# Performance work log

Measured on AMD Instinct MI355X. Metric: run time of the kernel, lower is better.

The kernel has to match this reference:

```python
import jax, jax.numpy as jnp
import numpy as np

B, N, DIM = 4, 4096, 512
HEADS, DH = 8, 64          # dim_head = dim // 8
M = 256                    # num_landmarks = dim // 2
ITERS = 6                  # pinv iterations
K = 33                     # residual depthwise conv kernel
INNER = HEADS * DH


def setup_inputs() -> dict:
    key = jax.random.key(0)
    ks = jax.random.split(key, 7)
    return {
        "x": jax.random.normal(ks[0], (B, N, DIM), jnp.float32),
        "norm_w": 1.0 + 0.02 * jax.random.normal(ks[1], (DIM,), jnp.float32),
        "norm_b": 0.02 * jax.random.normal(ks[2], (DIM,), jnp.float32),
        "w_qkv": jax.random.normal(ks[3], (DIM, 3 * INNER), jnp.float32) / np.sqrt(DIM),
        "w_out": jax.random.normal(ks[4], (INNER, DIM), jnp.float32) / np.sqrt(INNER),
        "b_out": 0.02 * jax.random.normal(ks[5], (DIM,), jnp.float32),
        "res_w": jax.random.normal(ks[6], (HEADS, 1, K, 1), jnp.float32) / np.sqrt(K),
    }


def _moore_penrose_pinv(x, iters):
    # iterative Newton-Schulz pseudoinverse, as in lucidrains nystrom-attention
    abs_x = jnp.abs(x)
    col = abs_x.sum(-1)
    row = abs_x.sum(-2)
    z = jnp.swapaxes(x, -1, -2) / (jnp.max(col) * jnp.max(row))
    I = jnp.eye(x.shape[-1], dtype=x.dtype)
    for _ in range(iters):
        xz = x @ z
        z = 0.25 * z @ (13.0 * I - xz @ (15.0 * I - xz @ (7.0 * I - xz)))
    return z


def reference(x, norm_w, norm_b, w_qkv, w_out, b_out, res_w):
    # LayerNorm (eps=1e-5, torch default)
    mu = x.mean(-1, keepdims=True)
    var = ((x - mu) ** 2).mean(-1, keepdims=True)
    xn = (x - mu) / jnp.sqrt(var + 1e-5) * norm_w + norm_b

    qkv = xn @ w_qkv                               # [B,N,3*INNER]
    q, k, v = jnp.split(qkv, 3, axis=-1)
    to_heads = lambda t: t.reshape(B, N, HEADS, DH).transpose(0, 2, 1, 3)  # [B,H,N,D]
    q, k, v = to_heads(q), to_heads(k), to_heads(v)
    q = q * (DH ** -0.5)

    # landmarks: mean over consecutive blocks of l = N // M tokens
    l = N // M
    q_l = q.reshape(B, HEADS, M, l, DH).mean(3)    # [B,H,M,D]
    k_l = k.reshape(B, HEADS, M, l, DH).mean(3)

    sim1 = jnp.einsum('bhid,bhjd->bhij', q, k_l)   # [B,H,N,M]
    sim2 = jnp.einsum('bhid,bhjd->bhij', q_l, k_l) # [B,H,M,M]
    sim3 = jnp.einsum('bhid,bhjd->bhij', q_l, k)   # [B,H,M,N]
    a1 = jax.nn.softmax(sim1, -1)
    a2 = jax.nn.softmax(sim2, -1)
    a3 = jax.nn.softmax(sim3, -1)

    a2_inv = _moore_penrose_pinv(a2, ITERS)
    out = (a1 @ a2_inv) @ (a3 @ v)                 # [B,H,N,D]

    # residual depthwise conv over sequence dim (Conv2d(h,h,(33,1),groups=h))
    out = out + jax.lax.conv_general_dilated(
        v, res_w, (1, 1), ((K // 2, K // 2), (0, 0)),
        feature_group_count=HEADS,
        dimension_numbers=('NCHW', 'OIHW', 'NCHW'))

    out = out.transpose(0, 2, 1, 3).reshape(B, N, INNER)
    out = out @ w_out + b_out                      # to_out (dropout inactive at eval)
    return x + out                                 # TransLayer residual
```

## Files before the change

### kernel.cpp

```cpp
#include <hip/hip_runtime.h>
#include <math.h>

typedef unsigned short u16;
typedef short s16x8 __attribute__((ext_vector_type(8)));
typedef float f32x4 __attribute__((ext_vector_type(4)));

#define MFMA16(a, b, c) __builtin_amdgcn_mfma_f32_16x16x32_bf16((a), (b), (c), 0, 0, 0)

__device__ __forceinline__ u16 f2b(float f) {
  unsigned u = __float_as_uint(f);
  unsigned r = (u + 0x7fff + ((u >> 16) & 1)) >> 16;
  return (u16)r;
}
__device__ __forceinline__ float b2f(u16 h) { return __uint_as_float(((unsigned)h) << 16); }

__global__ __launch_bounds__(256) void ln_kernel(const float* __restrict__ x, const float* __restrict__ w,
                          const float* __restrict__ b, u16* __restrict__ xn) {
  int row = blockIdx.x;
  const float* xr = x + (size_t)row * 512;
  int t = threadIdx.x;
  float v0 = xr[t], v1 = xr[t + 256];
  float s = v0 + v1, ss = v0*v0 + v1*v1;
  for (int o = 32; o > 0; o >>= 1) { s += __shfl_down(s, o); ss += __shfl_down(ss, o); }
  __shared__ float ls[4], lss[4];
  int wid = t >> 6, lane = t & 63;
  if (lane == 0) { ls[wid] = s; lss[wid] = ss; }
  __syncthreads();
  float tot  = ls[0]+ls[1]+ls[2]+ls[3];
  float tot2 = lss[0]+lss[1]+lss[2]+lss[3];
  float mean = tot * (1.f/512);
  float var  = tot2 * (1.f/512) - mean*mean;
  float inv = rsqrtf(var + 1e-5f);
  u16* xo = xn + (size_t)row * 512;
  xo[t]     = f2b((v0-mean)*inv*w[t]     + b[t]);
  xo[t+256] = f2b((v1-mean)*inv*w[t+256] + b[t+256]);
}

__global__ __launch_bounds__(256) void wcast_T(const float* __restrict__ W, u16* __restrict__ WT, int R, int C) {
  int idx = blockIdx.x*256 + threadIdx.x;
  if (idx >= R*C) return;
  int r = idx / C, c = idx - r*C;
  WT[(size_t)c*R + r] = f2b(W[idx]);
}

__global__ __launch_bounds__(256) void vtrans(const u16* __restrict__ v, u16* __restrict__ vT) {
  __shared__ u16 tile[64][72];
  int bh = blockIdx.y, n0 = blockIdx.x * 64;
  int t = threadIdx.x;
  const u16* vb = v + ((size_t)bh*4096 + n0)*64;
  #pragma unroll
  for (int p = 0; p < 2; p++) {
    int c = t + p*256;
    int r = c >> 3, col = (c & 7)*8;
    *(uint4*)&tile[r][col] = *(const uint4*)&vb[(size_t)r*64 + col];
  }
  __syncthreads();
  #pragma unroll
  for (int p = 0; p < 2; p++) {
    int c = t + p*256;
    int d = c >> 3, ncol = (c & 7)*8;
    u16 tmp[8];
    #pragma unroll
    for (int j = 0; j < 8; j++) tmp[j] = tile[ncol + j][d];
    *(uint4*)&vT[((size_t)bh*64 + d)*4096 + n0 + ncol] = *(uint4*)tmp;
  }
}

__device__ __forceinline__ void gemm128_core(const u16* __restrict__ A, const u16* __restrict__ BT,
    int K, int ldA, int ldBT, int row0, int col0, u16* As, u16* Bs, f32x4 acc[4][4]) {
  int t = threadIdx.x, lane = t & 63, wid = t >> 6;
  int wr = (wid >> 1) * 64, wc = (wid & 1) * 64;
  int lr = lane & 15, lg = lane >> 4;
  for (int k0 = 0; k0 < K; k0 += 32) {
    __syncthreads();
    #pragma unroll
    for (int p = 0; p < 2; p++) {
      int ch = t + p*256;
      int r = ch >> 2, c = (ch & 3) * 8;
      *(uint4*)&As[r*40 + c] = *(const uint4*)&A[(size_t)(row0 + r)*ldA + k0 + c];
      *(uint4*)&Bs[r*40 + c] = *(const uint4*)&BT[(size_t)(col0 + r)*ldBT + k0 + c];
    }
    __syncthreads();
    s16x8 af[4], bf[4];
    #pragma unroll
    for (int f = 0; f < 4; f++) {
      af[f] = *(s16x8*)&As[(wr + f*16 + lr)*40 + lg*8];
      bf[f] = *(s16x8*)&Bs[(wc + f*16 + lr)*40 + lg*8];
    }
    #pragma unroll
    for (int i = 0; i < 4; i++)
      #pragma unroll
      for (int j = 0; j < 4; j++)
        acc[i][j] = MFMA16(af[i], bf[j], acc[i][j]);
  }
}

__device__ __forceinline__ void gemm_128x64_core(const u16* __restrict__ A, const u16* __restrict__ BT,
    int row0, int col0, u16* As, u16* Bs, f32x4 acc[4][2]) {
  int t = threadIdx.x, lane = t & 63, wid = t >> 6;
  int wr = (wid >> 1) * 64, wc = (wid & 1) * 32;
  int lr = lane & 15, lg = lane >> 4;
  for (int k0 = 0; k0 < 256; k0 += 32) {
    __syncthreads();
    #pragma unroll
    for (int p = 0; p < 2; p++) {
      int ch = t + p*256;
      int r = ch >> 2, c = (ch & 3) * 8;
      *(uint4*)&As[r*40 + c] = *(const uint4*)&A[(size_t)(row0 + r)*256 + k0 + c];
    }
    { int r = t >> 2, c = (t & 3) * 8;
      *(uint4*)&Bs[r*40 + c] = *(const uint4*)&BT[(size_t)(col0 + r)*256 + k0 + c]; }
    __syncthreads();
    s16x8 af[4], bf[2];
    #pragma unroll
    for (int f = 0; f < 4; f++) af[f] = *(s16x8*)&As[(wr + f*16 + lr)*40 + lg*8];
    #pragma unroll
    for (int f = 0; f < 2; f++) bf[f] = *(s16x8*)&Bs[(wc + f*16 + lr)*40 + lg*8];
    #pragma unroll
    for (int i = 0; i < 4; i++)
      #pragma unroll
      for (int j = 0; j < 2; j++)
        acc[i][j] = MFMA16(af[i], bf[j], acc[i][j]);
  }
}

__global__ __launch_bounds__(256) void qkv_mfma(const u16* __restrict__ xn, const u16* __restrict__ wT,
    u16* __restrict__ q, u16* __restrict__ k, u16* __restrict__ v) {
  __shared__ u16 As[128*40], Bs[128*40];
  f32x4 acc[4][4];
  #pragma unroll
  for (int i = 0; i < 4; i++)
    #pragma unroll
    for (int j = 0; j < 4; j++) acc[i][j] = (f32x4)0.f;
  int bI = blockIdx.x;
  int job = (bI & 7)*192 + (bI >> 3);
  int row0 = (job / 12) * 128, col0 = (job % 12) * 128;
  gemm128_core(xn, wT, 512, 512, 512, row0, col0, As, Bs, acc);
  int t = threadIdx.x, lane = t & 63, wid = t >> 6, lr = lane & 15, lg = lane >> 4;
  int wr = (wid >> 1)*64, wc = (wid & 1)*64;
  #pragma unroll
  for (int i = 0; i < 4; i++)
    #pragma unroll
    for (int j = 0; j < 4; j++)
      #pragma unroll
      for (int r = 0; r < 4; r++) {
        int row = row0 + wr + i*16 + lg*4 + r;
        int col = col0 + wc + j*16 + lr;
        float val = acc[i][j][r];
        int part = col >> 9, rem = col & 511, h = rem >> 6, d = rem & 63;
        int b = row >> 12, n = row & 4095;
        size_t bh = (size_t)(b*8 + h);
        size_t dst = (bh*4096 + n)*64 + d;
        if (part == 0)      q[dst] = f2b(val * 0.125f);
        else if (part == 1) k[dst] = f2b(val);
        else                v[dst] = f2b(val);
      }
}

__global__ __launch_bounds__(256) void out_mfma(const u16* __restrict__ outh, const u16* __restrict__ wT,
    const float* __restrict__ bo, const float* __restrict__ x, float* __restrict__ out) {
  __shared__ u16 As[128*40], Bs[128*40];
  f32x4 acc[4][4];
  #pragma unroll
  for (int i = 0; i < 4; i++)
    #pragma unroll
    for (int j = 0; j < 4; j++) acc[i][j] = (f32x4)0.f;
  int bI = blockIdx.x;
  int job = (bI & 7)*64 + (bI >> 3);
  int row0 = (job / 4) * 128, col0 = (job % 4) * 128;
  gemm128_core(outh, wT, 512, 512, 512, row0, col0, As, Bs, acc);
  int t = threadIdx.x, lane = t & 63, wid = t >> 6, lr = lane & 15, lg = lane >> 4;
  int wr = (wid >> 1)*64, wc = (wid & 1)*64;
  #pragma unroll
  for (int i = 0; i < 4; i++)
    #pragma unroll
    for (int j = 0; j < 4; j++)
      #pragma unroll
      for (int r = 0; r < 4; r++) {
        int row = row0 + wr + i*16 + lg*4 + r;
        int col = col0 + wc + j*16 + lr;
        size_t idx = (size_t)row*512 + col;
        out[idx] = x[idx] + acc[i][j][r] + bo[col];
      }
}

__global__ __launch_bounds__(256) void pinv_s1(const u16* __restrict__ a2h, const u16* __restrict__ zcT,
    u16* __restrict__ xz, u16* __restrict__ xzT, u16* __restrict__ e1T) {
  __shared__ u16 As[128*40], Bs[64*40];
  size_t bb = (size_t)blockIdx.z << 16;
  f32x4 acc[4][2];
  #pragma unroll
  for (int i = 0; i < 4; i++) { acc[i][0] = (f32x4)0.f; acc[i][1] = (f32x4)0.f; }
  int row0 = blockIdx.y*128, col0 = blockIdx.x*64;
  gemm_128x64_core(a2h + bb, zcT + bb, row0, col0, As, Bs, acc);
  int t = threadIdx.x, lane = t & 63, wid = t >> 6, lr = lane & 15, lg = lane >> 4;
  int wr = (wid >> 1)*64, wc = (wid & 1)*32;
  #pragma unroll
  for (int i = 0; i < 4; i++)
    #pragma unroll
    for (int j = 0; j < 2; j++)
      #pragma unroll
      for (int r = 0; r < 4; r++) {
        int row = row0 + wr + i*16 + lg*4 + r;
        int col = col0 + wc + j*16 + lr;
        float c = acc[i][j][r];
        xz [bb + (size_t)row*256 + col] = f2b(c);
        xzT[bb + (size_t)col*256 + row] = f2b(c);
        e1T[bb + (size_t)col*256 + row] = f2b((row == col ? 7.f : 0.f) - c);
      }
}

__global__ __launch_bounds__(256) void pinv_s2(const u16* __restrict__ xz, const u16* __restrict__ e1T,
    const u16* __restrict__ zc, const u16* __restrict__ xzT,
    u16* __restrict__ e2T, u16* __restrict__ W) {
  __shared__ u16 As[128*40], Bs[64*40];
  int bz = blockIdx.z;
  bool isQ = bz < 32;
  size_t bb = (size_t)(isQ ? bz : bz - 32) << 16;
  const u16* Aptr = (isQ ? xz : zc) + bb;
  const u16* Bptr = (isQ ? e1T : xzT) + bb;
  f32x4 acc[4][2];
  #pragma unroll
  for (int i = 0; i < 4; i++) { acc[i][0] = (f32x4)0.f; acc[i][1] = (f32x4)0.f; }
  int row0 = blockIdx.y*128, col0 = blockIdx.x*64;
  gemm_128x64_core(Aptr, Bptr, row0, col0, As, Bs, acc);
  int t = threadIdx.x, lane = t & 63, wid = t >> 6, lr = lane & 15, lg = lane >> 4;
  int wr = (wid >> 1)*64, wc = (wid & 1)*32;
  #pragma unroll
  for (int i = 0; i < 4; i++)
    #pragma unroll
    for (int j = 0; j < 2; j++)
      #pragma unroll
      for (int r = 0; r < 4; r++) {
        int row = row0 + wr + i*16 + lg*4 + r;
        int col = col0 + wc + j*16 + lr;
        float c = acc[i][j][r];
        if (isQ) e2T[bb + (size_t)col*256 + row] = f2b((row == col ? 15.f : 0.f) - c);
        else     W  [bb + (size_t)row*256 + col] = f2b(c);
      }
}

__global__ __launch_bounds__(256) void pinv_s3(const u16* __restrict__ W, const u16* __restrict__ e2T,
    const u16* __restrict__ zc, u16* __restrict__ zn, u16* __restrict__ znT) {
  __shared__ u16 As[128*40], Bs[64*40];
  size_t bb = (size_t)blockIdx.z << 16;
  f32x4 acc[4][2];
  #pragma unroll
  for (int i = 0; i < 4; i++) { acc[i][0] = (f32x4)0.f; acc[i][1] = (f32x4)0.f; }
  int row0 = blockIdx.y*128, col0 = blockIdx.x*64;
  gemm_128x64_core(W + bb, e2T + bb, row0, col0, As, Bs, acc);
  int t = threadIdx.x, lane = t & 63, wid = t >> 6, lr = lane & 15, lg = lane >> 4;
  int wr = (wid >> 1)*64, wc = (wid & 1)*32;
  #pragma unroll
  for (int i = 0; i < 4; i++)
    #pragma unroll
    for (int j = 0; j < 2; j++)
      #pragma unroll
      for (int r = 0; r < 4; r++) {
        int row = row0 + wr + i*16 + lg*4 + r;
        int col = col0 + wc + j*16 + lr;
        size_t idx = bb + (size_t)row*256 + col;
        float val = 3.25f*b2f(zc[idx]) - 0.25f*acc[i][j][r];
        zn [idx] = f2b(val);
        znT[bb + (size_t)col*256 + row] = f2b(val);
      }
}

__global__ __launch_bounds__(256) void bmm64(const u16* __restrict__ A, const u16* __restrict__ BT,
    u16* __restrict__ Cn, u16* __restrict__ CT, u16* __restrict__ CE,
    int M, int N, int K, float alpha, float diag) {
  __shared__ u16 As[64*40], Bs[64*40];
  int batch = blockIdx.z;
  const u16* Ab = A  + (size_t)batch*M*K;
  const u16* Bb = BT + (size_t)batch*N*K;
  int row0 = blockIdx.y*64, col0 = blockIdx.x*64;
  int t = threadIdx.x, lane = t & 63, wid = t >> 6, lr = lane & 15, lg = lane >> 4;
  int wr = (wid >> 1)*32, wc = (wid & 1)*32;
  f32x4 acc[2][2];
  #pragma unroll
  for (int i = 0; i < 2; i++)
    #pragma unroll
    for (int j = 0; j < 2; j++) acc[i][j] = (f32x4)0.f;
  for (int k0 = 0; k0 < K; k0 += 32) {
    __syncthreads();
    int r = t >> 2, c = (t & 3)*8;
    *(uint4*)&As[r*40 + c] = *(const uint4*)&Ab[(size_t)(row0 + r)*K + k0 + c];
    *(uint4*)&Bs[r*40 + c] = *(const uint4*)&Bb[(size_t)(col0 + r)*K + k0 + c];
    __syncthreads();
    s16x8 af[2], bf[2];
    #pragma unroll
    for (int f = 0; f < 2; f++) {
      af[f] = *(s16x8*)&As[(wr + f*16 + lr)*40 + lg*8];
      bf[f] = *(s16x8*)&Bs[(wc + f*16 + lr)*40 + lg*8];
    }
    #pragma unroll
    for (int i = 0; i < 2; i++)
      #pragma unroll
      for (int j = 0; j < 2; j++)
        acc[i][j] = MFMA16(af[i], bf[j], acc[i][j]);
  }
  size_t cb = (size_t)batch*M*N;
  #pragma unroll
  for (int i = 0; i < 2; i++)
    #pragma unroll
    for (int j = 0; j < 2; j++)
      #pragma unroll
      for (int r = 0; r < 4; r++) {
        int row = row0 + wr + i*16 + lg*4 + r;
        int col = col0 + wc + j*16 + lr;
        float val = alpha*acc[i][j][r] + (row == col ? diag : 0.f);
        if (Cn) Cn[cb + (size_t)row*N + col] = f2b(val);
        if (CT) CT[cb + (size_t)col*M + row] = f2b(val);
        if (CE) CE[cb + (size_t)col*M + row] = f2b((row == col ? 7.f : 0.f) - val);
      }
}

__global__ void landmark_kernel(const u16* __restrict__ q, const u16* __restrict__ k,
                                u16* __restrict__ ql, u16* __restrict__ kl) {
  int idx = blockIdx.x;
  int d = threadIdx.x;
  size_t base = ((size_t)idx * 16) * 64 + d;
  float sq = 0.f, sk = 0.f;
  #pragma unroll
  for (int j = 0; j < 16; j++) { sq += b2f(q[base + (size_t)j*64]); sk += b2f(k[base + (size_t)j*64]); }
  ql[(size_t)idx*64 + d] = f2b(sq * (1.f/16.f));
  kl[(size_t)idx*64 + d] = f2b(sk * (1.f/16.f));
}

__global__ __launch_bounds__(256) void sim2_mfma(const u16* __restrict__ ql, const u16* __restrict__ kl,
    float* __restrict__ a2, u16* __restrict__ a2h, unsigned* __restrict__ scal) {
  __shared__ u16 Qs[256*72];
  __shared__ u16 Ks2[256*72];
  __shared__ float wcol[4*256];
  __shared__ float red[256];
  int bh = blockIdx.x;
  int t = threadIdx.x, lane = t & 63, wid = t >> 6, lr = lane & 15, lg = lane >> 4;
  #pragma unroll
  for (int p = 0; p < 8; p++) {
    int c = t + p*256;
    int r = c >> 3, col = (c & 7)*8;
    *(uint4*)&Qs[r*72 + col]  = *(const uint4*)&ql[((size_t)bh*256 + r)*64 + col];
    *(uint4*)&Ks2[r*72 + col] = *(const uint4*)&kl[((size_t)bh*256 + r)*64 + col];
  }
  __syncthreads();
  float colp[16];
  #pragma unroll
  for (int cf = 0; cf < 16; cf++) colp[cf] = 0.f;
  for (int rf = 0; rf < 4; rf++) {
    int rbase = wid*64 + rf*16;
    s16x8 a0 = *(s16x8*)&Qs[(rbase + lr)*72 + lg*8];
    s16x8 a1 = *(s16x8*)&Qs[(rbase + lr)*72 + 32 + lg*8];
    f32x4 sf[16];
    #pragma unroll
    for (int cf = 0; cf < 16; cf++) {
      s16x8 b0 = *(s16x8*)&Ks2[(cf*16 + lr)*72 + lg*8];
      s16x8 b1 = *(s16x8*)&Ks2[(cf*16 + lr)*72 + 32 + lg*8];
      sf[cf] = MFMA16(a1, b1, MFMA16(a0, b0, (f32x4)0.f));
    }
    #pragma unroll
    for (int r = 0; r < 4; r++) {
      float mx = -3e38f;
      #pragma unroll
      for (int cf = 0; cf < 16; cf++) mx = fmaxf(mx, sf[cf][r]);
      #pragma unroll
      for (int o = 1; o < 16; o <<= 1) mx = fmaxf(mx, __shfl_xor(mx, o));
      float sum = 0.f;
      #pragma unroll
      for (int cf = 0; cf < 16; cf++) { sf[cf][r] = __expf(sf[cf][r] - mx); sum += sf[cf][r]; }
      #pragma unroll
      for (int o = 1; o < 16; o <<= 1) sum += __shfl_xor(sum, o);
      float inv = 1.f / sum;
      int row = rbase + lg*4 + r;
      size_t base = (size_t)bh*65536 + (size_t)row*256;
      #pragma unroll
      for (int cf = 0; cf < 16; cf++) {
        float pp = sf[cf][r] * inv;
        a2[base + cf*16 + lr] = pp;
        a2h[base + cf*16 + lr] = f2b(pp);
        colp[cf] += pp;
      }
    }
  }
  #pragma unroll
  for (int cf = 0; cf < 16; cf++) {
    colp[cf] += __shfl_xor(colp[cf], 16);
    colp[cf] += __shfl_xor(colp[cf], 32);
  }
  if (lg == 0) {
    #pragma unroll
    for (int cf = 0; cf < 16; cf++) wcol[wid*256 + cf*16 + lr] = colp[cf];
  }
  __syncthreads();
  red[t] = wcol[t] + wcol[256 + t] + wcol[512 + t] + wcol[768 + t];
  __syncthreads();
  for (int o = 128; o > 0; o >>= 1) {
    if (t < o) red[t] = fmaxf(red[t], red[t+o]);
    __syncthreads();
  }
  if (t == 0) atomicMax(scal + 1, __float_as_uint(red[0]));
}

__global__ void z0_kernel(const float* __restrict__ a2, const unsigned* __restrict__ scal,
                          u16* __restrict__ zA, u16* __restrict__ zAT) {
  size_t idx = (size_t)blockIdx.x*256 + threadIdx.x;
  float inv = 1.f / __uint_as_float(scal[1]);
  size_t bh = idx >> 16; int rem = (int)(idx & 65535); int i = rem >> 8, j = rem & 255;
  zA[idx]  = f2b(a2[(bh<<16) + ((size_t)j<<8) + i] * inv);
  zAT[idx] = f2b(a2[idx] * inv);
}

__global__ __launch_bounds__(256) void flash_part(const u16* __restrict__ Q, const u16* __restrict__ Kg,
    const u16* __restrict__ VT, float* __restrict__ po, float* __restrict__ pm, float* __restrict__ pl) {
  __shared__ u16 Ks[64*72];
  __shared__ u16 Vs[64*72];
  __shared__ u16 Ps[4*16*72];
  int qt = blockIdx.x, ch = blockIdx.y, bh = blockIdx.z;
  int q0 = qt * 64;
  int t = threadIdx.x, lane = t & 63, wid = t >> 6, lr = lane & 15, lg = lane >> 4;
  const u16* Qb  = Q  + ((size_t)bh*256)*64;
  const u16* Kb  = Kg + ((size_t)bh*4096 + ch*512)*64;
  const u16* VTb = VT + ((size_t)bh*64)*4096 + ch*512;
  int qrow = q0 + wid*16 + lr;
  s16x8 aq0 = *(const s16x8*)&Qb[(size_t)qrow*64 + lg*8];
  s16x8 aq1 = *(const s16x8*)&Qb[(size_t)qrow*64 + 32 + lg*8];
  f32x4 oacc[4];
  #pragma unroll
  for (int f = 0; f < 4; f++) oacc[f] = (f32x4)0.f;
  float m_[4] = {-3e38f, -3e38f, -3e38f, -3e38f};
  float l_[4] = {0.f, 0.f, 0.f, 0.f};
  u16* Pw = Ps + wid*16*72;
  for (int k0 = 0; k0 < 512; k0 += 64) {
    __syncthreads();
    #pragma unroll
    for (int p = 0; p < 2; p++) {
      int c = t + p*256; int r = c >> 3, cc = (c & 7)*8;
      *(uint4*)&Ks[r*72 + cc] = *(const uint4*)&Kb[(size_t)(k0 + r)*64 + cc];
      *(uint4*)&Vs[r*72 + cc] = *(const uint4*)&VTb[(size_t)r*4096 + k0 + cc];
    }
    __syncthreads();
    f32x4 sf[4];
    #pragma unroll
    for (int f = 0; f < 4; f++) {
      s16x8 b0 = *(s16x8*)&Ks[(f*16 + lr)*72 + lg*8];
      s16x8 b1 = *(s16x8*)&Ks[(f*16 + lr)*72 + 32 + lg*8];
      f32x4 s = (f32x4)0.f;
      s = MFMA16(aq0, b0, s);
      s = MFMA16(aq1, b1, s);
      sf[f] = s;
    }
    #pragma unroll
    for (int r = 0; r < 4; r++) {
      float mx = fmaxf(fmaxf(sf[0][r], sf[1][r]), fmaxf(sf[2][r], sf[3][r]));
      #pragma unroll
      for (int o = 1; o < 16; o <<= 1) mx = fmaxf(mx, __shfl_xor(mx, o));
      float mn = fmaxf(m_[r], mx);
      float sum = 0.f;
      #pragma unroll
      for (int f = 0; f < 4; f++) {
        float pv = __expf(sf[f][r] - mn);
        sum += pv;
        Pw[(lg*4 + r)*72 + f*16 + lr] = f2b(pv);
      }
      #pragma unroll
      for (int o = 1; o < 16; o <<= 1) sum += __shfl_xor(sum, o);
      float sc = __expf(m_[r] - mn);
      l_[r] = l_[r]*sc + sum;
      m_[r] = mn;
      #pragma unroll
      for (int f = 0; f < 4; f++) oacc[f][r] *= sc;
    }
    __syncthreads();
    #pragma unroll
    for (int ks = 0; ks < 2; ks++) {
      s16x8 ap = *(s16x8*)&Pw[lr*72 + ks*32 + lg*8];
      #pragma unroll
      for (int df = 0; df < 4; df++) {
        s16x8 bv = *(s16x8*)&Vs[(df*16 + lr)*72 + ks*32 + lg*8];
        oacc[df] = MFMA16(ap, bv, oacc[df]);
      }
    }
  }
  int pidx = (bh*4 + qt)*8 + ch;
  #pragma unroll
  for (int r = 0; r < 4; r++) {
    int lrow = wid*16 + lg*4 + r;
    if (lr == 0) { pm[pidx*64 + lrow] = m_[r]; pl[pidx*64 + lrow] = l_[r]; }
    #pragma unroll
    for (int df = 0; df < 4; df++)
      po[((size_t)pidx*64 + lrow)*64 + df*16 + lr] = oacc[df][r];
  }
}

__global__ __launch_bounds__(256) void flash_merge(const float* __restrict__ po, const float* __restrict__ pm,
    const float* __restrict__ pl, u16* __restrict__ a3vT) {
  int row = blockIdx.x*4 + (threadIdx.x >> 6);
  int d = threadIdx.x & 63;
  int bh = row >> 8, qrow = row & 255, qt = qrow >> 6, lrow = qrow & 63;
  int pbase = (bh*4 + qt)*8;
  float m = -3e38f;
  #pragma unroll
  for (int ch = 0; ch < 8; ch++) m = fmaxf(m, pm[(pbase+ch)*64 + lrow]);
  float L = 0.f, O = 0.f;
  #pragma unroll
  for (int ch = 0; ch < 8; ch++) {
    float w = __expf(pm[(pbase+ch)*64 + lrow] - m);
    L += w * pl[(pbase+ch)*64 + lrow];
    O += w * po[((size_t)(pbase+ch)*64 + lrow)*64 + d];
  }
  a3vT[((size_t)bh*64 + d)*256 + qrow] = f2b(O / L);
}

__global__ __launch_bounds__(256) void flash_a1(const u16* __restrict__ Q, const u16* __restrict__ Kl,
    const u16* __restrict__ W2T, u16* __restrict__ outh) {
  __shared__ u16 Ks[64*72];
  __shared__ u16 Vs[64*264];
  __shared__ u16 Ps[4*16*264];
  int bh = blockIdx.y;
  int q0 = blockIdx.x * 64;
  int t = threadIdx.x, lane = t & 63, wid = t >> 6, lr = lane & 15, lg = lane >> 4;
  const u16* Qb = Q + ((size_t)bh*4096)*64;
  #pragma unroll
  for (int p = 0; p < 8; p++) {
    int c = t + p*256; int r = c >> 5, col = (c & 31)*8;
    *(uint4*)&Vs[r*264 + col] = *(const uint4*)&W2T[((size_t)bh*64 + r)*256 + col];
  }
  int qrow = q0 + wid*16 + lr;
  s16x8 aq0 = *(const s16x8*)&Qb[(size_t)qrow*64 + lg*8];
  s16x8 aq1 = *(const s16x8*)&Qb[(size_t)qrow*64 + 32 + lg*8];
  f32x4 sf[16];
  #pragma unroll
  for (int f = 0; f < 16; f++) sf[f] = (f32x4)0.f;
  #pragma unroll
  for (int kt = 0; kt < 4; kt++) {
    __syncthreads();
    #pragma unroll
    for (int p = 0; p < 2; p++) {
      int c = t + p*256; int r = c >> 3, cc = (c & 7)*8;
      *(uint4*)&Ks[r*72 + cc] = *(const uint4*)&Kl[((size_t)bh*256 + kt*64 + r)*64 + cc];
    }
    __syncthreads();
    #pragma unroll
    for (int f2 = 0; f2 < 4; f2++) {
      s16x8 b0 = *(s16x8*)&Ks[(f2*16 + lr)*72 + lg*8];
      s16x8 b1 = *(s16x8*)&Ks[(f2*16 + lr)*72 + 32 + lg*8];
      sf[kt*4 + f2] = MFMA16(aq1, b1, MFMA16(aq0, b0, sf[kt*4 + f2]));
    }
  }
  u16* Pw = Ps + wid*16*264;
  float linv[4];
  #pragma unroll
  for (int r = 0; r < 4; r++) {
    float mx = -3e38f;
    #pragma unroll
    for (int f = 0; f < 16; f++) mx = fmaxf(mx, sf[f][r]);
    #pragma unroll
    for (int o = 1; o < 16; o <<= 1) mx = fmaxf(mx, __shfl_xor(mx, o));
    float sum = 0.f;
    #pragma unroll
    for (int f = 0; f < 16; f++) {
      float pv = __expf(sf[f][r] - mx);
      sum += pv;
      Pw[(lg*4 + r)*264 + f*16 + lr] = f2b(pv);
    }
    #pragma unroll
    for (int o = 1; o < 16; o <<= 1) sum += __shfl_xor(sum, o);
    linv[r] = 1.f / sum;
  }
  f32x4 oacc[4];
  #pragma unroll
  for (int f = 0; f < 4; f++) oacc[f] = (f32x4)0.f;
  #pragma unroll
  for (int ks = 0; ks < 8; ks++) {
    s16x8 ap = *(s16x8*)&Pw[lr*264 + ks*32 + lg*8];
    #pragma unroll
    for (int df = 0; df < 4; df++) {
      s16x8 bv = *(s16x8*)&Vs[(df*16 + lr)*264 + ks*32 + lg*8];
      oacc[df] = MFMA16(ap, bv, oacc[df]);
    }
  }
  int b = bh >> 3, h = bh & 7;
  #pragma unroll
  for (int df = 0; df < 4; df++)
    #pragma unroll
    for (int r = 0; r < 4; r++) {
      int lrow = wid*16 + lg*4 + r;
      int col = df*16 + lr;
      outh[((size_t)(b*4096 + q0 + lrow))*512 + h*64 + col] = f2b(oacc[df][r] * linv[r]);
    }
}

__global__ __launch_bounds__(256) void conv_lds(const u16* __restrict__ v, const float* __restrict__ rw,
                                                u16* __restrict__ outh) {
  __shared__ u16 tile[160*72];
  __shared__ float wsm[33];
  int bh = blockIdx.y;
  int n0 = blockIdx.x * 128;
  int b = bh >> 3, h = bh & 7;
  int t = threadIdx.x;
  if (t < 33) wsm[t] = rw[h*33 + t];
  const u16* vb = v + ((size_t)bh*4096)*64;
  #pragma unroll
  for (int p = 0; p < 5; p++) {
    int c = t + p*256;
    int r = c >> 3, col = (c & 7)*8;
    int nn = n0 - 16 + r;
    uint4 val = make_uint4(0u,0u,0u,0u);
    if (nn >= 0 && nn < 4096) val = *(const uint4*)&vb[(size_t)nn*64 + col];
    *(uint4*)&tile[r*72 + col] = val;
  }
  __syncthreads();
  int d8 = (t & 7) * 8;
  int r0 = t >> 3;
  #pragma unroll
  for (int pass = 0; pass < 4; pass++) {
    int lrow = pass*32 + r0;
    float acc[8] = {};
    #pragma unroll
    for (int j = 0; j < 33; j++) {
      uint4 vv = *(uint4*)&tile[(lrow + j)*72 + d8];
      float w = wsm[j];
      acc[0] += b2f((u16)(vv.x & 0xffff)) * w;
      acc[1] += b2f((u16)(vv.x >> 16))    * w;
      acc[2] += b2f((u16)(vv.y & 0xffff)) * w;
      acc[3] += b2f((u16)(vv.y >> 16))    * w;
      acc[4] += b2f((u16)(vv.z & 0xffff)) * w;
      acc[5] += b2f((u16)(vv.z >> 16))    * w;
      acc[6] += b2f((u16)(vv.w & 0xffff)) * w;
      acc[7] += b2f((u16)(vv.w >> 16))    * w;
    }
    size_t oi = ((size_t)(b*4096 + n0 + lrow))*512 + h*64 + d8;
    uint4 ov = *(uint4*)&outh[oi];
    uint4 nv;
    nv.x = (unsigned)f2b(b2f((u16)(ov.x & 0xffff)) + acc[0]) | ((unsigned)f2b(b2f((u16)(ov.x >> 16)) + acc[1]) << 16);
    nv.y = (unsigned)f2b(b2f((u16)(ov.y & 0xffff)) + acc[2]) | ((unsigned)f2b(b2f((u16)(ov.y >> 16)) + acc[3]) << 16);
    nv.z = (unsigned)f2b(b2f((u16)(ov.z & 0xffff)) + acc[4]) | ((unsigned)f2b(b2f((u16)(ov.z >> 16)) + acc[5]) << 16);
    nv.w = (unsigned)f2b(b2f((u16)(ov.w & 0xffff)) + acc[6]) | ((unsigned)f2b(b2f((u16)(ov.w >> 16)) + acc[7]) << 16);
    *(uint4*)&outh[oi] = nv;
  }
}

extern "C" void kernel_launch(void* const* d_in, const int* in_sizes, int n_in,
                              void* d_out, int out_size, void* d_ws, size_t ws_size,
                              hipStream_t stream) {
  const float* x      = (const float*)d_in[0];
  const float* norm_w = (const float*)d_in[1];
  const float* norm_b = (const float*)d_in[2];
  const float* w_qkv  = (const float*)d_in[3];
  const float* w_out  = (const float*)d_in[4];
  const float* b_out  = (const float*)d_in[5];
  const float* res_w  = (const float*)d_in[6];
  float* out = (float*)d_out;
  char* ws = (char*)d_ws;

  size_t off = 0;
  u16* xn    = (u16*)(ws + off); off += 16777216;
  u16* q     = (u16*)(ws + off); off += 16777216;
  u16* k     = (u16*)(ws + off); off += 16777216;
  u16* v     = (u16*)(ws + off); off += 16777216;
  u16* vT    = (u16*)(ws + off); off += 16777216;
  u16* ql    = (u16*)(ws + off); off += 1048576;
  u16* kl    = (u16*)(ws + off); off += 1048576;
  float* a2  = (float*)(ws + off); off += 8388608;
  u16* a2h   = (u16*)(ws + off); off += 4194304;
  u16* zA    = (u16*)(ws + off); off += 4194304;
  u16* zAT   = (u16*)(ws + off); off += 4194304;
  u16* zB    = (u16*)(ws + off); off += 4194304;
  u16* zBT   = (u16*)(ws + off); off += 4194304;
  u16* xz    = (u16*)(ws + off); off += 4194304;
  u16* xzT   = (u16*)(ws + off); off += 4194304;
  u16* e1T   = (u16*)(ws + off); off += 4194304;
  u16* e2T   = (u16*)(ws + off); off += 4194304;
  u16* Wm    = (u16*)(ws + off); off += 4194304;
  u16* a3vT  = (u16*)(ws + off); off += 1048576;
  u16* w2T   = (u16*)(ws + off); off += 1048576;
  u16* wqkvT = (u16*)(ws + off); off += 1572864;
  u16* woutT = (u16*)(ws + off); off += 524288;
  u16* outh  = (u16*)(ws + off); off += 16777216;
  float* po  = (float*)(ws + off); off += 16777216;
  float* pm  = (float*)(ws + off); off += 262144;
  float* pl  = (float*)(ws + off); off += 262144;
  unsigned* scal = (unsigned*)(ws + off); off += 8;

  ln_kernel<<<16384, 256, 0, stream>>>(x, norm_w, norm_b, xn);
  wcast_T<<<3072, 256, 0, stream>>>(w_qkv, wqkvT, 512, 1536);
  wcast_T<<<1024, 256, 0, stream>>>(w_out, woutT, 512, 512);
  qkv_mfma<<<1536, 256, 0, stream>>>(xn, wqkvT, q, k, v);
  vtrans<<<dim3(64, 32), 256, 0, stream>>>(v, vT);
  landmark_kernel<<<8192, 64, 0, stream>>>(q, k, ql, kl);
  hipMemsetAsync(scal, 0, 8, stream);
  sim2_mfma<<<32, 256, 0, stream>>>(ql, kl, a2, a2h, scal);
  flash_part<<<dim3(4, 8, 32), 256, 0, stream>>>(ql, k, vT, po, pm, pl);
  flash_merge<<<2048, 256, 0, stream>>>(po, pm, pl, a3vT);
  z0_kernel<<<8192, 256, 0, stream>>>(a2, scal, zA, zAT);

  u16 *zc = zA, *zcT = zAT, *zn = zB, *znT = zBT;
  for (int it = 0; it < 6; it++) {
    pinv_s1<<<dim3(4,2,32), 256, 0, stream>>>(a2h, zcT, xz, xzT, e1T);
    pinv_s2<<<dim3(4,2,64), 256, 0, stream>>>(xz, e1T, zc, xzT, e2T, Wm);
    pinv_s3<<<dim3(4,2,32), 256, 0, stream>>>(Wm, e2T, zc, zn, znT);
    u16* tp;
    tp = zc; zc = zn; zn = tp;
    tp = zcT; zcT = znT; znT = tp;
  }

  bmm64<<<dim3(1,4,32), 256, 0, stream>>>(zc, a3vT, nullptr, w2T, nullptr, 256, 64, 256, 1.f, 0.f);
  flash_a1<<<dim3(64, 32), 256, 0, stream>>>(q, kl, w2T, outh);
  conv_lds<<<dim3(32, 32), 256, 0, stream>>>(v, res_w, outh);
  out_mfma<<<512, 256, 0, stream>>>(outh, woutT, b_out, x, out);
}
```

Before: 473.1 us.

## Add register prefetch to GEMM loops, shrink pinv tiles, split sim2 across blocks

Every GEMM core (qkv/out, pinv stages, bmm64) and flash_part now loads the next K-slice into registers while MFMAs run on the current LDS tile, so global-load latency is hidden. The pinv stages change from 128x64 to 64x64 tiles, which doubles the block count for the small 256x256 batched matmuls. sim2 now runs over 4 row chunks per head instead of one block per head, and a separate colmax kernel reduces the partial column sums. flash_part also drops one redundant barrier. The cost is higher register pressure and one extra kernel launch.

```diff
diff --git a/kernel.cpp b/kernel.cpp
--- a/kernel.cpp
+++ b/kernel.cpp
@@ -66,21 +66,31 @@
   }
 }
 
-__device__ __forceinline__ void gemm128_core(const u16* __restrict__ A, const u16* __restrict__ BT,
+__device__ __forceinline__ void gemm128_pf(const u16* __restrict__ A, const u16* __restrict__ BT,
     int K, int ldA, int ldBT, int row0, int col0, u16* As, u16* Bs, f32x4 acc[4][4]) {
   int t = threadIdx.x, lane = t & 63, wid = t >> 6;
   int wr = (wid >> 1) * 64, wc = (wid & 1) * 64;
   int lr = lane & 15, lg = lane >> 4;
+  int sr = t >> 2, sc = (t & 3) * 8;
+  const u16* Ar0 = A  + (size_t)(row0 + sr)*ldA + sc;
+  const u16* Ar1 = A  + (size_t)(row0 + sr + 64)*ldA + sc;
+  const u16* Br0 = BT + (size_t)(col0 + sr)*ldBT + sc;
+  const u16* Br1 = BT + (size_t)(col0 + sr + 64)*ldBT + sc;
+  uint4 pa0 = *(const uint4*)Ar0, pa1 = *(const uint4*)Ar1;
+  uint4 pb0 = *(const uint4*)Br0, pb1 = *(const uint4*)Br1;
   for (int k0 = 0; k0 < K; k0 += 32) {
     __syncthreads();
-    #pragma unroll
-    for (int p = 0; p < 2; p++) {
-      int ch = t + p*256;
-      int r = ch >> 2, c = (ch & 3) * 8;
-      *(uint4*)&As[r*40 + c] = *(const uint4*)&A[(size_t)(row0 + r)*ldA + k0 + c];
-      *(uint4*)&Bs[r*40 + c] = *(const uint4*)&BT[(size_t)(col0 + r)*ldBT + k0 + c];
-    }
-    __syncthreads();
+    *(uint4*)&As[sr*40 + sc]        = pa0;
+    *(uint4*)&As[(sr + 64)*40 + sc] = pa1;
+    *(uint4*)&Bs[sr*40 + sc]        = pb0;
+    *(uint4*)&Bs[(sr + 64)*40 + sc] = pb1;
+    __syncthreads();
+    if (k0 + 32 < K) {
+      pa0 = *(const uint4*)(Ar0 + k0 + 32);
+      pa1 = *(const uint4*)(Ar1 + k0 + 32);
+      pb0 = *(const uint4*)(Br0 + k0 + 32);
+      pb1 = *(const uint4*)(Br1 + k0 + 32);
+    }
     s16x8 af[4], bf[4];
     #pragma unroll
     for (int f = 0; f < 4; f++) {
@@ -95,29 +105,33 @@
   }
 }
 
-__device__ __forceinline__ void gemm_128x64_core(const u16* __restrict__ A, const u16* __restrict__ BT,
-    int row0, int col0, u16* As, u16* Bs, f32x4 acc[4][2]) {
+__device__ __forceinline__ void gemm64_pf(const u16* __restrict__ Ab, const u16* __restrict__ Bb,
+    int row0, int col0, u16* As, u16* Bs, f32x4 acc[2][2]) {
   int t = threadIdx.x, lane = t & 63, wid = t >> 6;
-  int wr = (wid >> 1) * 64, wc = (wid & 1) * 32;
+  int wr = (wid >> 1)*32, wc = (wid & 1)*32;
   int lr = lane & 15, lg = lane >> 4;
+  int sr = t >> 2, sc = (t & 3)*8;
+  const u16* Arow = Ab + (size_t)(row0 + sr)*256 + sc;
+  const u16* Brow = Bb + (size_t)(col0 + sr)*256 + sc;
+  uint4 pa = *(const uint4*)Arow;
+  uint4 pb = *(const uint4*)Brow;
   for (int k0 = 0; k0 < 256; k0 += 32) {
     __syncthreads();
-    #pragma unroll
-    for (int p = 0; p < 2; p++) {
-      int ch = t + p*256;
-      int r = ch >> 2, c = (ch & 3) * 8;
-      *(uint4*)&As[r*40 + c] = *(const uint4*)&A[(size_t)(row0 + r)*256 + k0 + c];
-    }
-    { int r = t >> 2, c = (t & 3) * 8;
-      *(uint4*)&Bs[r*40 + c] = *(const uint4*)&BT[(size_t)(col0 + r)*256 + k0 + c]; }
-    __syncthreads();
-    s16x8 af[4], bf[2];
-    #pragma unroll
-    for (int f = 0; f < 4; f++) af[f] = *(s16x8*)&As[(wr + f*16 + lr)*40 + lg*8];
-    #pragma unroll
-    for (int f = 0; f < 2; f++) bf[f] = *(s16x8*)&Bs[(wc + f*16 + lr)*40 + lg*8];
-    #pragma unroll
-    for (int i = 0; i < 4; i++)
+    *(uint4*)&As[sr*40 + sc] = pa;
+    *(uint4*)&Bs[sr*40 + sc] = pb;
+    __syncthreads();
+    if (k0 + 32 < 256) {
+      pa = *(const uint4*)(Arow + k0 + 32);
+      pb = *(const uint4*)(Brow + k0 + 32);
+    }
+    s16x8 af[2], bf[2];
+    #pragma unroll
+    for (int f = 0; f < 2; f++) {
+      af[f] = *(s16x8*)&As[(wr + f*16 + lr)*40 + lg*8];
+      bf[f] = *(s16x8*)&Bs[(wc + f*16 + lr)*40 + lg*8];
+    }
+    #pragma unroll
+    for (int i = 0; i < 2; i++)
       #pragma unroll
       for (int j = 0; j < 2; j++)
         acc[i][j] = MFMA16(af[i], bf[j], acc[i][j]);
@@ -135,7 +149,7 @@
   int bI = blockIdx.x;
   int job = (bI & 7)*192 + (bI >> 3);
   int row0 = (job / 12) * 128, col0 = (job % 12) * 128;
-  gemm128_core(xn, wT, 512, 512, 512, row0, col0, As, Bs, acc);
+  gemm128_pf(xn, wT, 512, 512, 512, row0, col0, As, Bs, acc);
   int t = threadIdx.x, lane = t & 63, wid = t >> 6, lr = lane & 15, lg = lane >> 4;
   int wr = (wid >> 1)*64, wc = (wid & 1)*64;
   #pragma unroll
@@ -168,7 +182,7 @@
   int bI = blockIdx.x;
   int job = (bI & 7)*64 + (bI >> 3);
   int row0 = (job / 4) * 128, col0 = (job % 4) * 128;
-  gemm128_core(outh, wT, 512, 512, 512, row0, col0, As, Bs, acc);
+  gemm128_pf(outh, wT, 512, 512, 512, row0, col0, As, Bs, acc);
   int t = threadIdx.x, lane = t & 63, wid = t >> 6, lr = lane & 15, lg = lane >> 4;
   int wr = (wid >> 1)*64, wc = (wid & 1)*64;
   #pragma unroll
@@ -186,17 +200,17 @@
 
 __global__ __launch_bounds__(256) void pinv_s1(const u16* __restrict__ a2h, const u16* __restrict__ zcT,
     u16* __restrict__ xz, u16* __restrict__ xzT, u16* __restrict__ e1T) {
-  __shared__ u16 As[128*40], Bs[64*40];
+  __shared__ u16 As[64*40], Bs[64*40];
   size_t bb = (size_t)blockIdx.z << 16;
-  f32x4 acc[4][2];
-  #pragma unroll
-  for (int i = 0; i < 4; i++) { acc[i][0] = (f32x4)0.f; acc[i][1] = (f32x4)0.f; }
-  int row0 = blockIdx.y*128, col0 = blockIdx.x*64;
-  gemm_128x64_core(a2h + bb, zcT + bb, row0, col0, As, Bs, acc);
-  int t = threadIdx.x, lane = t & 63, wid = t >> 6, lr = lane & 15, lg = lane >> 4;
-  int wr = (wid >> 1)*64, wc = (wid & 1)*32;
-  #pragma unroll
-  for (int i = 0; i < 4; i++)
+  f32x4 acc[2][2];
+  #pragma unroll
+  for (int i = 0; i < 2; i++) { acc[i][0] = (f32x4)0.f; acc[i][1] = (f32x4)0.f; }
+  int row0 = blockIdx.y*64, col0 = blockIdx.x*64;
+  gemm64_pf(a2h + bb, zcT + bb, row0, col0, As, Bs, acc);
+  int t = threadIdx.x, lane = t & 63, wid = t >> 6, lr = lane & 15, lg = lane >> 4;
+  int wr = (wid >> 1)*32, wc = (wid & 1)*32;
+  #pragma unroll
+  for (int i = 0; i < 2; i++)
     #pragma unroll
     for (int j = 0; j < 2; j++)
       #pragma unroll
@@ -213,21 +227,21 @@
 __global__ __launch_bounds__(256) void pinv_s2(const u16* __restrict__ xz, const u16* __restrict__ e1T,
     const u16* __restrict__ zc, const u16* __restrict__ xzT,
     u16* __restrict__ e2T, u16* __restrict__ W) {
-  __shared__ u16 As[128*40], Bs[64*40];
+  __shared__ u16 As[64*40], Bs[64*40];
   int bz = blockIdx.z;
   bool isQ = bz < 32;
   size_t bb = (size_t)(isQ ? bz : bz - 32) << 16;
   const u16* Aptr = (isQ ? xz : zc) + bb;
   const u16* Bptr = (isQ ? e1T : xzT) + bb;
-  f32x4 acc[4][2];
-  #pragma unroll
-  for (int i = 0; i < 4; i++) { acc[i][0] = (f32x4)0.f; acc[i][1] = (f32x4)0.f; }
-  int row0 = blockIdx.y*128, col0 = blockIdx.x*64;
-  gemm_128x64_core(Aptr, Bptr, row0, col0, As, Bs, acc);
-  int t = threadIdx.x, lane = t & 63, wid = t >> 6, lr = lane & 15, lg = lane >> 4;
-  int wr = (wid >> 1)*64, wc = (wid & 1)*32;
-  #pragma unroll
-  for (int i = 0; i < 4; i++)
+  f32x4 acc[2][2];
+  #pragma unroll
+  for (int i = 0; i < 2; i++) { acc[i][0] = (f32x4)0.f; acc[i][1] = (f32x4)0.f; }
+  int row0 = blockIdx.y*64, col0 = blockIdx.x*64;
+  gemm64_pf(Aptr, Bptr, row0, col0, As, Bs, acc);
+  int t = threadIdx.x, lane = t & 63, wid = t >> 6, lr = lane & 15, lg = lane >> 4;
+  int wr = (wid >> 1)*32, wc = (wid & 1)*32;
+  #pragma unroll
+  for (int i = 0; i < 2; i++)
     #pragma unroll
     for (int j = 0; j < 2; j++)
       #pragma unroll
@@ -242,17 +256,17 @@
 
 __global__ __launch_bounds__(256) void pinv_s3(const u16* __restrict__ W, const u16* __restrict__ e2T,
     const u16* __restrict__ zc, u16* __restrict__ zn, u16* __restrict__ znT) {
-  __shared__ u16 As[128*40], Bs[64*40];
+  __shared__ u16 As[64*40], Bs[64*40];
   size_t bb = (size_t)blockIdx.z << 16;
-  f32x4 acc[4][2];
-  #pragma unroll
-  for (int i = 0; i < 4; i++) { acc[i][0] = (f32x4)0.f; acc[i][1] = (f32x4)0.f; }
-  int row0 = blockIdx.y*128, col0 = blockIdx.x*64;
-  gemm_128x64_core(W + bb, e2T + bb, row0, col0, As, Bs, acc);
-  int t = threadIdx.x, lane = t & 63, wid = t >> 6, lr = lane & 15, lg = lane >> 4;
-  int wr = (wid >> 1)*64, wc = (wid & 1)*32;
-  #pragma unroll
-  for (int i = 0; i < 4; i++)
+  f32x4 acc[2][2];
+  #pragma unroll
+  for (int i = 0; i < 2; i++) { acc[i][0] = (f32x4)0.f; acc[i][1] = (f32x4)0.f; }
+  int row0 = blockIdx.y*64, col0 = blockIdx.x*64;
+  gemm64_pf(W + bb, e2T + bb, row0, col0, As, Bs, acc);
+  int t = threadIdx.x, lane = t & 63, wid = t >> 6, lr = lane & 15, lg = lane >> 4;
+  int wr = (wid >> 1)*32, wc = (wid & 1)*32;
+  #pragma unroll
+  for (int i = 0; i < 2; i++)
     #pragma unroll
     for (int j = 0; j < 2; j++)
       #pragma unroll
@@ -267,8 +281,7 @@
 }
 
 __global__ __launch_bounds__(256) void bmm64(const u16* __restrict__ A, const u16* __restrict__ BT,
-    u16* __restrict__ Cn, u16* __restrict__ CT, u16* __restrict__ CE,
-    int M, int N, int K, float alpha, float diag) {
+    u16* __restrict__ CT, int M, int N, int K) {
   __shared__ u16 As[64*40], Bs[64*40];
   int batch = blockIdx.z;
   const u16* Ab = A  + (size_t)batch*M*K;
@@ -276,6 +289,11 @@
   int row0 = blockIdx.y*64, col0 = blockIdx.x*64;
   int t = threadIdx.x, lane = t & 63, wid = t >> 6, lr = lane & 15, lg = lane >> 4;
   int wr = (wid >> 1)*32, wc = (wid & 1)*32;
+  int sr = t >> 2, sc = (t & 3)*8;
+  const u16* Arow = Ab + (size_t)(row0 + sr)*K + sc;
+  const u16* Brow = Bb + (size_t)(col0 + sr)*K + sc;
+  uint4 pa = *(const uint4*)Arow;
+  uint4 pb = *(const uint4*)Brow;
   f32x4 acc[2][2];
   #pragma unroll
   for (int i = 0; i < 2; i++)
@@ -283,10 +301,13 @@
     for (int j = 0; j < 2; j++) acc[i][j] = (f32x4)0.f;
   for (int k0 = 0; k0 < K; k0 += 32) {
     __syncthreads();
-    int r = t >> 2, c = (t & 3)*8;
-    *(uint4*)&As[r*40 + c] = *(const uint4*)&Ab[(size_t)(row0 + r)*K + k0 + c];
-    *(uint4*)&Bs[r*40 + c] = *(const uint4*)&Bb[(size_t)(col0 + r)*K + k0 + c];
-    __syncthreads();
+    *(uint4*)&As[sr*40 + sc] = pa;
+    *(uint4*)&Bs[sr*40 + sc] = pb;
+    __syncthreads();
+    if (k0 + 32 < K) {
+      pa = *(const uint4*)(Arow + k0 + 32);
+      pb = *(const uint4*)(Brow + k0 + 32);
+    }
     s16x8 af[2], bf[2];
     #pragma unroll
     for (int f = 0; f < 2; f++) {
@@ -308,10 +329,7 @@
       for (int r = 0; r < 4; r++) {
         int row = row0 + wr + i*16 + lg*4 + r;
         int col = col0 + wc + j*16 + lr;
-        float val = alpha*acc[i][j][r] + (row == col ? diag : 0.f);
-        if (Cn) Cn[cb + (size_t)row*N + col] = f2b(val);
-        if (CT) CT[cb + (size_t)col*M + row] = f2b(val);
-        if (CE) CE[cb + (size_t)col*M + row] = f2b((row == col ? 7.f : 0.f) - val);
+        CT[cb + (size_t)col*M + row] = f2b(acc[i][j][r]);
       }
 }
 
@@ -328,57 +346,59 @@
 }
 
 __global__ __launch_bounds__(256) void sim2_mfma(const u16* __restrict__ ql, const u16* __restrict__ kl,
-    float* __restrict__ a2, u16* __restrict__ a2h, unsigned* __restrict__ scal) {
-  __shared__ u16 Qs[256*72];
+    float* __restrict__ a2, u16* __restrict__ a2h, float* __restrict__ pcs) {
+  __shared__ u16 Qs[64*72];
   __shared__ u16 Ks2[256*72];
   __shared__ float wcol[4*256];
-  __shared__ float red[256];
-  int bh = blockIdx.x;
-  int t = threadIdx.x, lane = t & 63, wid = t >> 6, lr = lane & 15, lg = lane >> 4;
+  int rq = blockIdx.x, bh = blockIdx.y;
+  int t = threadIdx.x, lane = t & 63, wid = t >> 6, lr = lane & 15, lg = lane >> 4;
+  #pragma unroll
+  for (int p = 0; p < 2; p++) {
+    int c = t + p*256;
+    int r = c >> 3, col = (c & 7)*8;
+    *(uint4*)&Qs[r*72 + col] = *(const uint4*)&ql[((size_t)bh*256 + rq*64 + r)*64 + col];
+  }
   #pragma unroll
   for (int p = 0; p < 8; p++) {
     int c = t + p*256;
     int r = c >> 3, col = (c & 7)*8;
-    *(uint4*)&Qs[r*72 + col]  = *(const uint4*)&ql[((size_t)bh*256 + r)*64 + col];
     *(uint4*)&Ks2[r*72 + col] = *(const uint4*)&kl[((size_t)bh*256 + r)*64 + col];
   }
   __syncthreads();
   float colp[16];
   #pragma unroll
   for (int cf = 0; cf < 16; cf++) colp[cf] = 0.f;
-  for (int rf = 0; rf < 4; rf++) {
-    int rbase = wid*64 + rf*16;
-    s16x8 a0 = *(s16x8*)&Qs[(rbase + lr)*72 + lg*8];
-    s16x8 a1 = *(s16x8*)&Qs[(rbase + lr)*72 + 32 + lg*8];
-    f32x4 sf[16];
+  int rbase = wid*16;
+  s16x8 a0 = *(s16x8*)&Qs[(rbase + lr)*72 + lg*8];
+  s16x8 a1 = *(s16x8*)&Qs[(rbase + lr)*72 + 32 + lg*8];
+  f32x4 sf[16];
+  #pragma unroll
+  for (int cf = 0; cf < 16; cf++) {
+    s16x8 b0 = *(s16x8*)&Ks2[(cf*16 + lr)*72 + lg*8];
+    s16x8 b1 = *(s16x8*)&Ks2[(cf*16 + lr)*72 + 32 + lg*8];
+    sf[cf] = MFMA16(a1, b1, MFMA16(a0, b0, (f32x4)0.f));
+  }
+  #pragma unroll
+  for (int r = 0; r < 4; r++) {
+    float mx = -3e38f;
+    #pragma unroll
+    for (int cf = 0; cf < 16; cf++) mx = fmaxf(mx, sf[cf][r]);
+    #pragma unroll
+    for (int o = 1; o < 16; o <<= 1) mx = fmaxf(mx, __shfl_xor(mx, o));
+    float sum = 0.f;
+    #pragma unroll
+    for (int cf = 0; cf < 16; cf++) { sf[cf][r] = __expf(sf[cf][r] - mx); sum += sf[cf][r]; }
+    #pragma unroll
+    for (int o = 1; o < 16; o <<= 1) sum += __shfl_xor(sum, o);
+    float inv = 1.f / sum;
+    int row = rq*64 + rbase + lg*4 + r;
+    size_t base = (size_t)bh*65536 + (size_t)row*256;
     #pragma unroll
     for (int cf = 0; cf < 16; cf++) {
-      s16x8 b0 = *(s16x8*)&Ks2[(cf*16 + lr)*72 + lg*8];
-      s16x8 b1 = *(s16x8*)&Ks2[(cf*16 + lr)*72 + 32 + lg*8];
-      sf[cf] = MFMA16(a1, b1, MFMA16(a0, b0, (f32x4)0.f));
-    }
-    #pragma unroll
-    for (int r = 0; r < 4; r++) {
-      float mx = -3e38f;
-      #pragma unroll
-      for (int cf = 0; cf < 16; cf++) mx = fmaxf(mx, sf[cf][r]);
-      #pragma unroll
-      for (int o = 1; o < 16; o <<= 1) mx = fmaxf(mx, __shfl_xor(mx, o));
-      float sum = 0.f;
-      #pragma unroll
-      for (int cf = 0; cf < 16; cf++) { sf[cf][r] = __expf(sf[cf][r] - mx); sum += sf[cf][r]; }
-      #pragma unroll
-      for (int o = 1; o < 16; o <<= 1) sum += __shfl_xor(sum, o);
-      float inv = 1.f / sum;
-      int row = rbase + lg*4 + r;
-      size_t base = (size_t)bh*65536 + (size_t)row*256;
-      #pragma unroll
-      for (int cf = 0; cf < 16; cf++) {
-        float pp = sf[cf][r] * inv;
-        a2[base + cf*16 + lr] = pp;
-        a2h[base + cf*16 + lr] = f2b(pp);
-        colp[cf] += pp;
-      }
+      float pp = sf[cf][r] * inv;
+      a2[base + cf*16 + lr] = pp;
+      a2h[base + cf*16 + lr] = f2b(pp);
+      colp[cf] += pp;
     }
   }
   #pragma unroll
@@ -391,7 +411,14 @@
     for (int cf = 0; cf < 16; cf++) wcol[wid*256 + cf*16 + lr] = colp[cf];
   }
   __syncthreads();
-  red[t] = wcol[t] + wcol[256 + t] + wcol[512 + t] + wcol[768 + t];
+  pcs[((size_t)bh*4 + rq)*256 + t] = wcol[t] + wcol[256 + t] + wcol[512 + t] + wcol[768 + t];
+}
+
+__global__ __launch_bounds__(256) void colmax_kernel(const float* __restrict__ pcs, unsigned* __restrict__ scal) {
+  __shared__ float red[256];
+  int bh = blockIdx.x, t = threadIdx.x;
+  size_t b4 = (size_t)bh*4*256;
+  red[t] = pcs[b4 + t] + pcs[b4 + 256 + t] + pcs[b4 + 512 + t] + pcs[b4 + 768 + t];
   __syncthreads();
   for (int o = 128; o > 0; o >>= 1) {
     if (t < o) red[t] = fmaxf(red[t], red[t+o]);
@@ -429,15 +456,30 @@
   float m_[4] = {-3e38f, -3e38f, -3e38f, -3e38f};
   float l_[4] = {0.f, 0.f, 0.f, 0.f};
   u16* Pw = Ps + wid*16*72;
+  uint4 pk[2], pv[2];
+  #pragma unroll
+  for (int p = 0; p < 2; p++) {
+    int c = t + p*256; int r = c >> 3, cc = (c & 7)*8;
+    pk[p] = *(const uint4*)&Kb[(size_t)r*64 + cc];
+    pv[p] = *(const uint4*)&VTb[(size_t)r*4096 + cc];
+  }
   for (int k0 = 0; k0 < 512; k0 += 64) {
     __syncthreads();
     #pragma unroll
     for (int p = 0; p < 2; p++) {
       int c = t + p*256; int r = c >> 3, cc = (c & 7)*8;
-      *(uint4*)&Ks[r*72 + cc] = *(const uint4*)&Kb[(size_t)(k0 + r)*64 + cc];
-      *(uint4*)&Vs[r*72 + cc] = *(const uint4*)&VTb[(size_t)r*4096 + k0 + cc];
-    }
-    __syncthreads();
+      *(uint4*)&Ks[r*72 + cc] = pk[p];
+      *(uint4*)&Vs[r*72 + cc] = pv[p];
+    }
+    __syncthreads();
+    if (k0 + 64 < 512) {
+      #pragma unroll
+      for (int p = 0; p < 2; p++) {
+        int c = t + p*256; int r = c >> 3, cc = (c & 7)*8;
+        pk[p] = *(const uint4*)&Kb[(size_t)(k0 + 64 + r)*64 + cc];
+        pv[p] = *(const uint4*)&VTb[(size_t)r*4096 + k0 + 64 + cc];
+      }
+    }
     f32x4 sf[4];
     #pragma unroll
     for (int f = 0; f < 4; f++) {
@@ -457,9 +499,9 @@
       float sum = 0.f;
       #pragma unroll
       for (int f = 0; f < 4; f++) {
-        float pv = __expf(sf[f][r] - mn);
-        sum += pv;
-        Pw[(lg*4 + r)*72 + f*16 + lr] = f2b(pv);
+        float pv2 = __expf(sf[f][r] - mn);
+        sum += pv2;
+        Pw[(lg*4 + r)*72 + f*16 + lr] = f2b(pv2);
       }
       #pragma unroll
       for (int o = 1; o < 16; o <<= 1) sum += __shfl_xor(sum, o);
@@ -469,7 +511,6 @@
       #pragma unroll
       for (int f = 0; f < 4; f++) oacc[f][r] *= sc;
     }
-    __syncthreads();
     #pragma unroll
     for (int ks = 0; ks < 2; ks++) {
       s16x8 ap = *(s16x8*)&Pw[lr*72 + ks*32 + lg*8];
@@ -679,6 +720,7 @@
   float* po  = (float*)(ws + off); off += 16777216;
   float* pm  = (float*)(ws + off); off += 262144;
   float* pl  = (float*)(ws + off); off += 262144;
+  float* pcs = (float*)(ws + off); off += 131072;
   unsigned* scal = (unsigned*)(ws + off); off += 8;
 
   ln_kernel<<<16384, 256, 0, stream>>>(x, norm_w, norm_b, xn);
@@ -688,22 +730,23 @@
   vtrans<<<dim3(64, 32), 256, 0, stream>>>(v, vT);
   landmark_kernel<<<8192, 64, 0, stream>>>(q, k, ql, kl);
   hipMemsetAsync(scal, 0, 8, stream);
-  sim2_mfma<<<32, 256, 0, stream>>>(ql, kl, a2, a2h, scal);
+  sim2_mfma<<<dim3(4, 32), 256, 0, stream>>>(ql, kl, a2, a2h, pcs);
+  colmax_kernel<<<32, 256, 0, stream>>>(pcs, scal);
   flash_part<<<dim3(4, 8, 32), 256, 0, stream>>>(ql, k, vT, po, pm, pl);
   flash_merge<<<2048, 256, 0, stream>>>(po, pm, pl, a3vT);
   z0_kernel<<<8192, 256, 0, stream>>>(a2, scal, zA, zAT);
 
   u16 *zc = zA, *zcT = zAT, *zn = zB, *znT = zBT;
   for (int it = 0; it < 6; it++) {
-    pinv_s1<<<dim3(4,2,32), 256, 0, stream>>>(a2h, zcT, xz, xzT, e1T);
-    pinv_s2<<<dim3(4,2,64), 256, 0, stream>>>(xz, e1T, zc, xzT, e2T, Wm);
-    pinv_s3<<<dim3(4,2,32), 256, 0, stream>>>(Wm, e2T, zc, zn, znT);
+    pinv_s1<<<dim3(4,4,32), 256, 0, stream>>>(a2h, zcT, xz, xzT, e1T);
+    pinv_s2<<<dim3(4,4,64), 256, 0, stream>>>(xz, e1T, zc, xzT, e2T, Wm);
+    pinv_s3<<<dim3(4,4,32), 256, 0, stream>>>(Wm, e2T, zc, zn, znT);
     u16* tp;
     tp = zc; zc = zn; zn = tp;
     tp = zcT; zcT = znT; znT = tp;
   }
 
-  bmm64<<<dim3(1,4,32), 256, 0, stream>>>(zc, a3vT, nullptr, w2T, nullptr, 256, 64, 256, 1.f, 0.f);
+  bmm64<<<dim3(1,4,32), 256, 0, stream>>>(zc, a3vT, w2T, 256, 64, 256);
   flash_a1<<<dim3(64, 32), 256, 0, stream>>>(q, kl, w2T, outh);
   conv_lds<<<dim3(32, 32), 256, 0, stream>>>(v, res_w, outh);
   out_mfma<<<512, 256, 0, stream>>>(outh, woutT, b_out, x, out);
```

Result: faster. 459.7 us (-2.8%).
